# Kernel tuning notes

Hardware: AMD Instinct MI355X
Metric: run time of the kernel (lower is better)

## Reference

```python
import jax, jax.numpy as jnp
import numpy as np

VOCAB, EMBED, HIDDEN = 32000, 512, 1024
BATCH, SRC_LEN = 64, 1024

def _xavier(key, shape):
    fan_out, fan_in = shape
    bound = float(np.sqrt(6.0 / (fan_in + fan_out)))
    return jax.random.uniform(key, shape, jnp.float32, -bound, bound)

def setup_inputs() -> dict:
    key = jax.random.key(0)
    k0, k1, k2, k3, k4 = jax.random.split(key, 5)
    src = jax.random.randint(k0, (BATCH, SRC_LEN), 0, VOCAB)
    emb = jax.random.normal(k1, (VOCAB, EMBED), jnp.float32)  # nn.Embedding default N(0,1)
    Wx = _xavier(k2, (4 * HIDDEN, EMBED))                     # x2h weight (out,in)
    bx = jax.random.uniform(k3, (4 * HIDDEN,), jnp.float32,
                            -1.0 / np.sqrt(EMBED), 1.0 / np.sqrt(EMBED))  # Linear default bias init
    Wh = _xavier(k4, (4 * HIDDEN, HIDDEN))                    # h2h weight, no bias
    return {"src": src, "emb": emb, "Wx": Wx, "bx": bx, "Wh": Wh}

def reference(src, emb, Wx, bx, Wh):
    B, T = src.shape
    H = Wh.shape[1]
    embedded = emb[src]                      # (B, T, E)
    # Precompute input projections for all steps: (T, B, 4H)
    x_proj = jnp.einsum('bte,ge->tbg', embedded, Wx) + bx

    def step(carry, xg):
        h, c = carry
        gates = xg + h @ Wh.T                # (B, 4H)
        i, f, o, g = jnp.split(gates, 4, axis=1)
        i = jax.nn.sigmoid(i)
        f = jax.nn.sigmoid(f)
        o = jax.nn.sigmoid(o)
        g = jnp.tanh(g)
        c = f * c + i * g
        h = o * jnp.tanh(c)
        return (h, c), None

    init = (jnp.zeros((B, H), jnp.float32), jnp.zeros((B, H), jnp.float32))
    (h_t, c_t), _ = jax.lax.scan(step, init, x_proj)
    return (h_t, c_t)
```

## Files before the change

kernel.cpp:

```cpp
#include <hip/hip_runtime.h>

typedef unsigned short u16;
typedef unsigned int   u32;
typedef unsigned long long u64;
typedef __attribute__((ext_vector_type(8))) __bf16 bf16x8;
typedef __attribute__((ext_vector_type(4))) float   f32x4;

#define B_   64
#define H_   1024
#define E_   512
#define G4_  4096
#define T_   1024
#define NWG  64

__device__ __forceinline__ u16 f2b(float f){
  union { float f; u32 u; } v; v.f = f;
  u32 r = v.u + 0x7fffu + ((v.u >> 16) & 1u);
  return (u16)(r >> 16);
}
__device__ __forceinline__ float b2f(u16 u){
  union { u32 u; float f; } v; v.u = ((u32)u) << 16;
  return v.f;
}
__device__ __forceinline__ float sigf(float x){
  return 1.0f / (1.0f + __expf(-x));
}
__device__ __forceinline__ float tanhf_s(float x){
  float ax = fabsf(x);
  float e  = __expf(2.0f * ax);
  float t  = 1.0f - 2.0f / (e + 1.0f);
  return copysignf(t, x);
}
__device__ __forceinline__ void gload_lds16(const void* g, void* l){
  __builtin_amdgcn_global_load_lds(
      (const __attribute__((address_space(1))) u32*)g,
      (__attribute__((address_space(3))) u32*)l, 16, 0, 0);
}

__global__ __launch_bounds__(256) void cvt_bf16(const float* __restrict__ in,
                                                u16* __restrict__ out, int n){
  int i = (blockIdx.x * 256 + threadIdx.x) * 4;
  if (i >= n) return;
  float4 v = *reinterpret_cast<const float4*>(in + i);
  ushort4 o;
  o.x = f2b(v.x); o.y = f2b(v.y); o.z = f2b(v.z); o.w = f2b(v.w);
  *reinterpret_cast<ushort4*>(out + i) = o;
}

__global__ __launch_bounds__(256) void emb_gather(const int* __restrict__ src,
                                                  const float* __restrict__ emb,
                                                  u16* __restrict__ embSeg, int t0){
  int idx = blockIdx.x * 256 + threadIdx.x;
  int m  = idx >> 7;
  int e4 = (idx & 127) << 2;
  int b = m & 63, ts = m >> 6;
  int tok = src[b * T_ + t0 + ts];
  float4 v = *reinterpret_cast<const float4*>(emb + (size_t)tok * E_ + e4);
  ushort4 o;
  o.x = f2b(v.x); o.y = f2b(v.y); o.z = f2b(v.z); o.w = f2b(v.w);
  *reinterpret_cast<ushort4*>(embSeg + (size_t)m * E_ + e4) = o;
}

__global__ __launch_bounds__(256) void xproj_gemm(const u16* __restrict__ embSeg,
                                                  const u16* __restrict__ WxB,
                                                  const float* __restrict__ bx,
                                                  u16* __restrict__ xp){
  __shared__ alignas(16) u16 Al[2][128][64];
  __shared__ alignas(16) u16 Bl[2][128][64];
  const int tid  = threadIdx.x;
  const int lane = tid & 63, wv = tid >> 6;
  const int wm = wv >> 1, wn = wv & 1;
  const int m0 = blockIdx.y * 128, n0 = blockIdx.x * 128;

  const int srow_w = wv * 8 + (lane >> 3);
  const int csrc   = (lane & 7) ^ (lane >> 3);

  auto stage = [&](int buf, int kb){
    const int kbase = kb * 64 + csrc * 8;
    #pragma unroll
    for (int it = 0; it < 4; ++it){
      const u16* ga = embSeg + (size_t)(m0 + it * 32 + srow_w) * E_ + kbase;
      gload_lds16(ga, &Al[buf][it * 32 + wv * 8][0]);
    }
    #pragma unroll
    for (int it = 0; it < 4; ++it){
      const u16* gb = WxB + (size_t)(n0 + it * 32 + srow_w) * E_ + kbase;
      gload_lds16(gb, &Bl[buf][it * 32 + wv * 8][0]);
    }
  };

  f32x4 acc[4][4] = {};
  stage(0, 0);
  __syncthreads();
  for (int kb = 0; kb < 8; ++kb){
    const int cur = kb & 1;
    if (kb < 7) stage(cur ^ 1, kb + 1);
    #pragma unroll
    for (int kk = 0; kk < 2; ++kk){
      bf16x8 af[4], bfr[4];
      #pragma unroll
      for (int i = 0; i < 4; ++i){
        int row = wm * 64 + i * 16 + (lane & 15);
        int cp  = (kk * 4 + (lane >> 4)) ^ (row & 7);
        af[i] = *reinterpret_cast<const bf16x8*>(&Al[cur][row][cp * 8]);
      }
      #pragma unroll
      for (int j = 0; j < 4; ++j){
        int row = wn * 64 + j * 16 + (lane & 15);
        int cp  = (kk * 4 + (lane >> 4)) ^ (row & 7);
        bfr[j] = *reinterpret_cast<const bf16x8*>(&Bl[cur][row][cp * 8]);
      }
      #pragma unroll
      for (int i = 0; i < 4; ++i)
        #pragma unroll
        for (int j = 0; j < 4; ++j)
          acc[i][j] = __builtin_amdgcn_mfma_f32_16x16x32_bf16(af[i], bfr[j], acc[i][j], 0, 0, 0);
    }
    __syncthreads();
  }

  float bxv[4];
  #pragma unroll
  for (int j = 0; j < 4; ++j) bxv[j] = bx[n0 + wn * 64 + j * 16 + (lane & 15)];
  #pragma unroll
  for (int i = 0; i < 4; ++i){
    int mrow = m0 + wm * 64 + i * 16 + ((lane >> 4) << 2);
    #pragma unroll
    for (int r = 0; r < 4; ++r){
      size_t base = (size_t)(mrow + r) * G4_ + n0 + wn * 64 + (lane & 15);
      #pragma unroll
      for (int j = 0; j < 4; ++j)
        xp[base + j * 16] = f2b(acc[i][j][r] + bxv[j]);
    }
  }
}

__global__ __launch_bounds__(256, 1) void lstm_rec(const float* __restrict__ Wh,
                                                   const u16* __restrict__ xp,
                                                   u16* __restrict__ hring,
                                                   float* __restrict__ c_state,
                                                   u32* __restrict__ cnt,
                                                   float* __restrict__ out,
                                                   int t0, int t1, int segm1){
  __shared__ alignas(16) u16 Wl[64][1024];
  const int tid  = threadIdx.x;
  const int lane = tid & 63, wv = tid >> 6;
  const int wg   = blockIdx.x;

  for (int it = tid; it < 64 * 128; it += 256){
    int r = it >> 7, c = it & 127;
    int gc = c ^ (r & 15);
    const float* gsrc = Wh + ((size_t)(r >> 4) * H_ + wg * 16 + (r & 15)) * H_ + gc * 8;
    float4 a = *reinterpret_cast<const float4*>(gsrc);
    float4 d = *reinterpret_cast<const float4*>(gsrc + 4);
    union { u16 s[8]; uint4 q; } u;
    u.s[0]=f2b(a.x); u.s[1]=f2b(a.y); u.s[2]=f2b(a.z); u.s[3]=f2b(a.w);
    u.s[4]=f2b(d.x); u.s[5]=f2b(d.y); u.s[6]=f2b(d.z); u.s[7]=f2b(d.w);
    *reinterpret_cast<uint4*>(&Wl[r][c * 8]) = u.q;
  }
  __syncthreads();

  const int b     = wv * 16 + (lane & 15);
  const int jbase = (lane >> 4) << 2;

  float cst[4];
  if (t0 == 0){
    cst[0] = cst[1] = cst[2] = cst[3] = 0.f;
  } else {
    float4 cv = *reinterpret_cast<const float4*>(c_state + (size_t)b * H_ + wg * 16 + jbase);
    cst[0] = cv.x; cst[1] = cv.y; cst[2] = cv.z; cst[3] = cv.w;
  }

  for (int t = t0; t < t1; ++t){
    const int ts = t - t0;
    ushort4 xv[4];
    const u16* xrow = xp + ((size_t)ts * B_ + b) * G4_ + wg * 16 + jbase;
    #pragma unroll
    for (int q = 0; q < 4; ++q)
      xv[q] = *reinterpret_cast<const ushort4*>(xrow + q * H_);

    f32x4 acc[4] = {};
    if (t > 0){
      const u32* cp = cnt + ((size_t)(t - 1) * 8 + (lane & 7)) * 16;
      while (__hip_atomic_load(cp, __ATOMIC_RELAXED, __HIP_MEMORY_SCOPE_AGENT) < 8u) { }
      asm volatile("" ::: "memory");

      const u16* hp = hring + (size_t)((t - 1) & segm1) * (B_ * H_)
                    + (size_t)b * H_ + ((lane >> 4) << 3);
      uint4 hq[32];
      #pragma unroll
      for (int ks = 0; ks < 32; ++ks)
        hq[ks] = *reinterpret_cast<const uint4*>(hp + ks * 32);

      f32x4 accA[4] = {}, accB[4] = {};
      #pragma unroll
      for (int ks = 0; ks < 16; ++ks){
        union { uint4 q; bf16x8 v; } u; u.q = hq[ks];
        #pragma unroll
        for (int m = 0; m < 4; ++m){
          int row = m * 16 + (lane & 15);
          int cp2 = (ks * 4 + (lane >> 4)) ^ (row & 15);
          bf16x8 aw = *reinterpret_cast<const bf16x8*>(&Wl[row][cp2 * 8]);
          accA[m] = __builtin_amdgcn_mfma_f32_16x16x32_bf16(aw, u.v, accA[m], 0, 0, 0);
        }
      }
      #pragma unroll
      for (int ks = 16; ks < 32; ++ks){
        union { uint4 q; bf16x8 v; } u; u.q = hq[ks];
        #pragma unroll
        for (int m = 0; m < 4; ++m){
          int row = m * 16 + (lane & 15);
          int cp2 = (ks * 4 + (lane >> 4)) ^ (row & 15);
          bf16x8 aw = *reinterpret_cast<const bf16x8*>(&Wl[row][cp2 * 8]);
          accB[m] = __builtin_amdgcn_mfma_f32_16x16x32_bf16(aw, u.v, accB[m], 0, 0, 0);
        }
      }
      #pragma unroll
      for (int m = 0; m < 4; ++m) acc[m] = accA[m] + accB[m];
    }

    float hv[4];
    #pragma unroll
    for (int r = 0; r < 4; ++r){
      u16 x0 = (r==0)?xv[0].x:(r==1)?xv[0].y:(r==2)?xv[0].z:xv[0].w;
      u16 x1 = (r==0)?xv[1].x:(r==1)?xv[1].y:(r==2)?xv[1].z:xv[1].w;
      u16 x2 = (r==0)?xv[2].x:(r==1)?xv[2].y:(r==2)?xv[2].z:xv[2].w;
      u16 x3 = (r==0)?xv[3].x:(r==1)?xv[3].y:(r==2)?xv[3].z:xv[3].w;
      float gi = sigf(acc[0][r] + b2f(x0));
      float gf = sigf(acc[1][r] + b2f(x1));
      float go = sigf(acc[2][r] + b2f(x2));
      float gg = tanhf_s(acc[3][r] + b2f(x3));
      cst[r] = (t == 0) ? gi * gg : gf * cst[r] + gi * gg;
      hv[r]  = go * tanhf_s(cst[r]);
    }

    if (t < T_ - 1){
      u64 pk =  (u64)f2b(hv[0])
             | ((u64)f2b(hv[1]) << 16)
             | ((u64)f2b(hv[2]) << 32)
             | ((u64)f2b(hv[3]) << 48);
      u64* hd = (u64*)(hring + (size_t)(t & segm1) * (B_ * H_)
                       + (size_t)b * H_ + wg * 16 + jbase);
      __hip_atomic_store(hd, pk, __ATOMIC_RELAXED, __HIP_MEMORY_SCOPE_AGENT);
      asm volatile("s_waitcnt vmcnt(0)" ::: "memory");
      __syncthreads();
      if (tid == 0)
        __hip_atomic_fetch_add(cnt + ((size_t)t * 8 + (wg >> 3)) * 16, 1u,
                               __ATOMIC_RELAXED, __HIP_MEMORY_SCOPE_AGENT);
    } else {
      float4 ho; ho.x = hv[0]; ho.y = hv[1]; ho.z = hv[2]; ho.w = hv[3];
      float4 co; co.x = cst[0]; co.y = cst[1]; co.z = cst[2]; co.w = cst[3];
      *reinterpret_cast<float4*>(out + (size_t)b * H_ + wg * 16 + jbase) = ho;
      *reinterpret_cast<float4*>(out + (size_t)(B_ * H_) + (size_t)b * H_ + wg * 16 + jbase) = co;
    }
  }

  if (t1 < T_){
    float4 cv; cv.x = cst[0]; cv.y = cst[1]; cv.z = cst[2]; cv.w = cst[3];
    *reinterpret_cast<float4*>(c_state + (size_t)b * H_ + wg * 16 + jbase) = cv;
  }
}

extern "C" void kernel_launch(void* const* d_in, const int* in_sizes, int n_in,
                              void* d_out, int out_size, void* d_ws, size_t ws_size,
                              hipStream_t stream){
  const int*   src = (const int*)  d_in[0];
  const float* emb = (const float*)d_in[1];
  const float* Wx  = (const float*)d_in[2];
  const float* bx  = (const float*)d_in[3];
  const float* Wh  = (const float*)d_in[4];

  const size_t FIXED  = 4194304 + 262144 + 524288;
  const size_t PERSEG = 65536 + 524288 + 131072;
  int SEG = 64;
  if (ws_size < FIXED + 64 * PERSEG){
    if      (ws_size >= FIXED + 16 * PERSEG) SEG = 16;
    else if (ws_size >= FIXED + 4  * PERSEG) SEG = 4;
    else                                     SEG = 2;
  }

  char*  ws      = (char*)d_ws;
  u16*   WxB     = (u16*)(ws);
  u16*   embSeg  = (u16*)(ws + 4194304);
  u16*   xpSeg   = (u16*)(ws + 4194304 + (size_t)SEG * 65536);
  u16*   hring   = (u16*)(ws + 4194304 + (size_t)SEG * 589824);
  float* c_state = (float*)(ws + 4194304 + (size_t)SEG * 720896);
  u32*   cnt     = (u32*) (ws + 4194304 + (size_t)SEG * 720896 + 262144);

  hipMemsetAsync(cnt, 0, (size_t)T_ * 8 * 64, stream);
  cvt_bf16<<<2048, 256, 0, stream>>>(Wx, WxB, G4_ * E_);

  const int nseg = T_ / SEG;
  for (int s = 0; s < nseg; ++s){
    const int t0   = s * SEG;
    const int rows = SEG * B_;
    emb_gather<<<rows / 2, 256, 0, stream>>>(src, emb, embSeg, t0);
    dim3 g(G4_ / 128, rows / 128);
    xproj_gemm<<<g, 256, 0, stream>>>(embSeg, WxB, bx, xpSeg);
    lstm_rec<<<NWG, 256, 0, stream>>>(Wh, xpSeg, hring, c_state, cnt,
                                      (float*)d_out, t0, t0 + SEG, SEG - 1);
  }
}
```

Measured before the change: 7.091 ms.

## Replace per-step counter barrier with per-wave byte flags and progressive h loads

The recurrent kernel's per-timestep sync is reworked. The block-wide __syncthreads plus one atomic counter increment per workgroup is replaced by a byte flag written per wave. Consumers poll these flags with a ballot and load each slice of h as soon as its producers are ready, so loads overlap the waiting. The h ring buffer is re-laid out so each workgroup's output is contiguous, and the default segment length doubles to cut kernel launches. The cost is more polling traffic and more complex flag decoding, with some risk of spin contention.

After: 9.994 ms. 1.41x slower.

```diff
diff --git a/kernel.cpp b/kernel.cpp
--- a/kernel.cpp
+++ b/kernel.cpp
@@ -1,6 +1,7 @@
 #include <hip/hip_runtime.h>
 
 typedef unsigned short u16;
+typedef unsigned char  u8;
 typedef unsigned int   u32;
 typedef unsigned long long u64;
 typedef __attribute__((ext_vector_type(8))) __bf16 bf16x8;
@@ -139,7 +140,7 @@
                                                    const u16* __restrict__ xp,
                                                    u16* __restrict__ hring,
                                                    float* __restrict__ c_state,
-                                                   u32* __restrict__ cnt,
+                                                   u8*  __restrict__ flags8,
                                                    float* __restrict__ out,
                                                    int t0, int t1, int segm1){
   __shared__ alignas(16) u16 Wl[64][1024];
@@ -161,7 +162,9 @@
   __syncthreads();
 
   const int b     = wv * 16 + (lane & 15);
-  const int jbase = (lane >> 4) << 2;
+  const int hi    = lane >> 4;
+  const int jbase = hi << 2;
+  const int hoff  = b * 16 + (hi >> 1) * 1024 + (hi & 1) * 8;
 
   float cst[4];
   if (t0 == 0){
@@ -181,16 +184,28 @@
 
     f32x4 acc[4] = {};
     if (t > 0){
-      const u32* cp = cnt + ((size_t)(t - 1) * 8 + (lane & 7)) * 16;
-      while (__hip_atomic_load(cp, __ATOMIC_RELAXED, __HIP_MEMORY_SCOPE_AGENT) < 8u) { }
-      asm volatile("" ::: "memory");
-
-      const u16* hp = hring + (size_t)((t - 1) & segm1) * (B_ * H_)
-                    + (size_t)b * H_ + ((lane >> 4) << 3);
+      const u16* hpb = hring + (size_t)((t - 1) & segm1) * (B_ * H_) + hoff;
+      const u32* flg = (const u32*)(flags8 + (size_t)(t - 1) * 256) + lane;
       uint4 hq[32];
-      #pragma unroll
-      for (int ks = 0; ks < 32; ++ks)
-        hq[ks] = *reinterpret_cast<const uint4*>(hp + ks * 32);
+      u32 seen = 0;
+      #pragma unroll
+      for (int g = 0; g < 8; ++g){
+        while (!((seen >> g) & 1u)){
+          u32 f = __hip_atomic_load(flg, __ATOMIC_RELAXED, __HIP_MEMORY_SCOPE_AGENT);
+          u64 bal = __ballot(f == 0x01010101u);
+          bal &= bal >> 4; bal &= bal >> 2; bal &= bal >> 1;
+          u32 m8 = (u32)(bal & 1)        | ((u32)(bal >> 7)  & 2)  | ((u32)(bal >> 14) & 4)
+                 | ((u32)(bal >> 21) & 8)| ((u32)(bal >> 28) & 16) | ((u32)(bal >> 35) & 32)
+                 | ((u32)(bal >> 42) & 64)| ((u32)(bal >> 49) & 128);
+          seen |= m8;
+          if (!((seen >> g) & 1u)) __builtin_amdgcn_s_sleep(1);
+        }
+        asm volatile("" ::: "memory");
+        hq[g * 4 + 0] = *reinterpret_cast<const uint4*>(hpb + (g * 4 + 0) * 2048);
+        hq[g * 4 + 1] = *reinterpret_cast<const uint4*>(hpb + (g * 4 + 1) * 2048);
+        hq[g * 4 + 2] = *reinterpret_cast<const uint4*>(hpb + (g * 4 + 2) * 2048);
+        hq[g * 4 + 3] = *reinterpret_cast<const uint4*>(hpb + (g * 4 + 3) * 2048);
+      }
 
       f32x4 accA[4] = {}, accB[4] = {};
       #pragma unroll
@@ -199,7 +214,7 @@
         #pragma unroll
         for (int m = 0; m < 4; ++m){
           int row = m * 16 + (lane & 15);
-          int cp2 = (ks * 4 + (lane >> 4)) ^ (row & 15);
+          int cp2 = (ks * 4 + hi) ^ (row & 15);
           bf16x8 aw = *reinterpret_cast<const bf16x8*>(&Wl[row][cp2 * 8]);
           accA[m] = __builtin_amdgcn_mfma_f32_16x16x32_bf16(aw, u.v, accA[m], 0, 0, 0);
         }
@@ -210,7 +225,7 @@
         #pragma unroll
         for (int m = 0; m < 4; ++m){
           int row = m * 16 + (lane & 15);
-          int cp2 = (ks * 4 + (lane >> 4)) ^ (row & 15);
+          int cp2 = (ks * 4 + hi) ^ (row & 15);
           bf16x8 aw = *reinterpret_cast<const bf16x8*>(&Wl[row][cp2 * 8]);
           accB[m] = __builtin_amdgcn_mfma_f32_16x16x32_bf16(aw, u.v, accB[m], 0, 0, 0);
         }
@@ -240,13 +255,12 @@
              | ((u64)f2b(hv[2]) << 32)
              | ((u64)f2b(hv[3]) << 48);
       u64* hd = (u64*)(hring + (size_t)(t & segm1) * (B_ * H_)
-                       + (size_t)b * H_ + wg * 16 + jbase);
+                       + wg * 1024 + b * 16 + jbase);
       __hip_atomic_store(hd, pk, __ATOMIC_RELAXED, __HIP_MEMORY_SCOPE_AGENT);
       asm volatile("s_waitcnt vmcnt(0)" ::: "memory");
-      __syncthreads();
-      if (tid == 0)
-        __hip_atomic_fetch_add(cnt + ((size_t)t * 8 + (wg >> 3)) * 16, 1u,
-                               __ATOMIC_RELAXED, __HIP_MEMORY_SCOPE_AGENT);
+      if (lane == 0)
+        __hip_atomic_store(flags8 + (size_t)t * 256 + wg * 4 + wv, (u8)1,
+                           __ATOMIC_RELAXED, __HIP_MEMORY_SCOPE_AGENT);
     } else {
       float4 ho; ho.x = hv[0]; ho.y = hv[1]; ho.z = hv[2]; ho.w = hv[3];
       float4 co; co.x = cst[0]; co.y = cst[1]; co.z = cst[2]; co.w = cst[3];
@@ -270,11 +284,12 @@
   const float* bx  = (const float*)d_in[3];
   const float* Wh  = (const float*)d_in[4];
 
-  const size_t FIXED  = 4194304 + 262144 + 524288;
+  const size_t FIXED  = 4194304 + 262144 + 262144;
   const size_t PERSEG = 65536 + 524288 + 131072;
-  int SEG = 64;
-  if (ws_size < FIXED + 64 * PERSEG){
-    if      (ws_size >= FIXED + 16 * PERSEG) SEG = 16;
+  int SEG = 128;
+  if (ws_size < FIXED + 128 * PERSEG){
+    if      (ws_size >= FIXED + 64 * PERSEG) SEG = 64;
+    else if (ws_size >= FIXED + 16 * PERSEG) SEG = 16;
     else if (ws_size >= FIXED + 4  * PERSEG) SEG = 4;
     else                                     SEG = 2;
   }
@@ -285,9 +300,9 @@
   u16*   xpSeg   = (u16*)(ws + 4194304 + (size_t)SEG * 65536);
   u16*   hring   = (u16*)(ws + 4194304 + (size_t)SEG * 589824);
   float* c_state = (float*)(ws + 4194304 + (size_t)SEG * 720896);
-  u32*   cnt     = (u32*) (ws + 4194304 + (size_t)SEG * 720896 + 262144);
-
-  hipMemsetAsync(cnt, 0, (size_t)T_ * 8 * 64, stream);
+  u8*    flags8  = (u8*)  (ws + 4194304 + (size_t)SEG * 720896 + 262144);
+
+  hipMemsetAsync(flags8, 0, (size_t)T_ * 256, stream);
   cvt_bf16<<<2048, 256, 0, stream>>>(Wx, WxB, G4_ * E_);
 
   const int nseg = T_ / SEG;
@@ -297,7 +312,7 @@
     emb_gather<<<rows / 2, 256, 0, stream>>>(src, emb, embSeg, t0);
     dim3 g(G4_ / 128, rows / 128);
     xproj_gemm<<<g, 256, 0, stream>>>(embSeg, WxB, bx, xpSeg);
-    lstm_rec<<<NWG, 256, 0, stream>>>(Wh, xpSeg, hring, c_state, cnt,
+    lstm_rec<<<NWG, 256, 0, stream>>>(Wh, xpSeg, hring, c_state, flags8,
                                       (float*)d_out, t0, t0 + SEG, SEG - 1);
   }
 }
```
